# Optimization experiments

Measured on AMD Instinct MI355X. Metric: run time of the kernel, lower is better.

The kernel has to match this reference:

```python
import jax, jax.numpy as jnp
import numpy as np
from jax import lax

D_MODEL = 512
KERNEL = 17
DILATION = 1
MLP_MULT = 4
EPS = 1e-6


def rmsnorm(x, w):
    # x: [B,T,C]; RMSNorm: x * rsqrt(mean(x^2) + eps) * w
    ms = jnp.mean(x * x, axis=-1, keepdims=True)
    return x * lax.rsqrt(ms + EPS) * w


def causal_dwconv(x, w, dilation):
    # x: [B,T,C], w: [C,K]. Equivalent math to the FFT path in the torch code:
    # y[b,t,c] = sum_k w[c,k] * x[b, t - dilation*(K-1) + dilation*k, c] (zeros off left edge)
    B, T, C = x.shape
    K = w.shape[1]
    left_pad = dilation * (K - 1)
    lhs = jnp.transpose(x, (0, 2, 1))          # [B,C,T]
    rhs = w[:, None, :]                        # [C,1,K] depthwise
    y = lax.conv_general_dilated(
        lhs, rhs,
        window_strides=(1,),
        padding=[(left_pad, 0)],
        rhs_dilation=(dilation,),
        dimension_numbers=('NCH', 'OIH', 'NCH'),
        feature_group_count=C,
    )                                          # [B,C,T]
    return jnp.transpose(y, (0, 2, 1))


def setup_inputs() -> dict:
    key = jax.random.key(0)
    ks = jax.random.split(key, 8)
    B, T, d = 4, 16384, D_MODEL
    h = MLP_MULT * d
    scale = lambda fan_in: 1.0 / np.sqrt(fan_in)
    return {
        'x': jax.random.normal(ks[0], (B, T, d), jnp.float32),
        'ln1_w': jnp.ones((d,), jnp.float32),
        'gate_w': jax.random.normal(ks[1], (d, d), jnp.float32) * scale(d),
        'conv_w': jax.random.uniform(ks[2], (d, KERNEL), jnp.float32,
                                     -scale(KERNEL), scale(KERNEL)),
        'proj_w': jax.random.normal(ks[3], (d, d), jnp.float32) * scale(d),
        'ln2_w': jnp.ones((d,), jnp.float32),
        'mlp_w1': jax.random.normal(ks[4], (d, h), jnp.float32) * scale(d),
        'mlp_w2': jax.random.normal(ks[5], (h, d), jnp.float32) * scale(h),
    }


def reference(x, ln1_w, gate_w, conv_w, proj_w, ln2_w, mlp_w1, mlp_w2):
    # Gated depthwise causal conv branch
    hn = rmsnorm(x, ln1_w)
    g = jax.nn.sigmoid(jnp.einsum('btd,de->bte', hn, gate_w))
    hc = causal_dwconv(hn, conv_w, DILATION)
    x = x + jnp.einsum('btd,de->bte', g * hc, proj_w)
    # MLP branch
    hn2 = rmsnorm(x, ln2_w)
    mid = jax.nn.gelu(jnp.einsum('btd,dh->bth', hn2, mlp_w1))
    x = x + jnp.einsum('bth,hd->btd', mid, mlp_w2)
    return x
```

## Files before the change

kernel.cpp:

```cpp
#include <hip/hip_runtime.h>
#include <hip/hip_bf16.h>
#include <cstdint>
#include <cstddef>

typedef __attribute__((ext_vector_type(8))) short short8;
typedef __attribute__((ext_vector_type(4))) short short4v;
typedef __attribute__((ext_vector_type(4))) float floatx4;

#define D_MODEL 512
#define HDIM    2048
#define TSEQ    16384
#define NTOK    65536

__device__ __forceinline__ float bf2f(short s) {
  union { unsigned u; float f; } v; v.u = ((unsigned)(unsigned short)s) << 16; return v.f;
}
__device__ __forceinline__ short f2bf(float f) {
  union { float fv; unsigned u; } v; v.fv = f;
  unsigned u = v.u;
  u += 0x7FFFu + ((u >> 16) & 1u);
  return (short)(u >> 16);
}
__device__ __forceinline__ void gload_lds16(const void* g, void* l) {
  __builtin_amdgcn_global_load_lds((const __attribute__((address_space(1))) void*)g,
                                   (__attribute__((address_space(3))) void*)l, 16, 0, 0);
}

__global__ void wt_transpose(const float* __restrict__ W, short* __restrict__ Wt,
                             const int K, const int N) {
  __shared__ float t[64][65];
  const int tid = threadIdx.x;
  const long k0 = (long)blockIdx.x * 64;
  const long n0 = (long)blockIdx.y * 64;
  const int rr = tid >> 4;
  const int cc = (tid & 15) * 4;
#pragma unroll
  for (int i = 0; i < 4; ++i) {
    const int r = rr + i * 16;
    const float4 v = *(const float4*)(W + (k0 + r) * N + n0 + cc);
    t[r][cc + 0] = v.x; t[r][cc + 1] = v.y; t[r][cc + 2] = v.z; t[r][cc + 3] = v.w;
  }
  __syncthreads();
#pragma unroll
  for (int i = 0; i < 4; ++i) {
    const int n = rr + i * 16;
    short4v o;
    o[0] = f2bf(t[cc + 0][n]);
    o[1] = f2bf(t[cc + 1][n]);
    o[2] = f2bf(t[cc + 2][n]);
    o[3] = f2bf(t[cc + 3][n]);
    *(short4v*)(Wt + (n0 + n) * K + k0 + cc) = o;
  }
}

__global__ void convw_transpose(const float* __restrict__ cw, float* __restrict__ wT) {
  const int idx = blockIdx.x * 256 + threadIdx.x;
  if (idx >= 17 * D_MODEL) return;
  const int k = idx / D_MODEL;
  const int c = idx % D_MODEL;
  wT[idx] = cw[c * 17 + k];
}

__global__ void rmsnorm_kernel(const float* __restrict__ x, const float* __restrict__ w,
                               short* __restrict__ outp) {
  const int lane = threadIdx.x & 63;
  const long row = (long)blockIdx.x * 4 + (threadIdx.x >> 6);
  const float* xr = x + row * D_MODEL + lane * 8;
  const float4 a = *(const float4*)xr;
  const float4 b = *(const float4*)(xr + 4);
  float ss = a.x * a.x + a.y * a.y + a.z * a.z + a.w * a.w
           + b.x * b.x + b.y * b.y + b.z * b.z + b.w * b.w;
#pragma unroll
  for (int m = 32; m; m >>= 1) ss += __shfl_xor(ss, m);
  const float scale = rsqrtf(ss * (1.0f / D_MODEL) + 1e-6f);
  const float4 wa = *(const float4*)(w + lane * 8);
  const float4 wb = *(const float4*)(w + lane * 8 + 4);
  short8 o;
  o[0] = f2bf(a.x * scale * wa.x);
  o[1] = f2bf(a.y * scale * wa.y);
  o[2] = f2bf(a.z * scale * wa.z);
  o[3] = f2bf(a.w * scale * wa.w);
  o[4] = f2bf(b.x * scale * wb.x);
  o[5] = f2bf(b.y * scale * wb.y);
  o[6] = f2bf(b.z * scale * wb.z);
  o[7] = f2bf(b.w * scale * wb.w);
  *(short8*)(outp + row * D_MODEL + lane * 8) = o;
}

__global__ void dwconv_kernel(const short* __restrict__ hn, const float* __restrict__ wT,
                              short* __restrict__ hc) {
  const int tid = threadIdx.x;
  const int chunk = tid & 63;
  const long row = (long)blockIdx.x * 4 + (tid >> 6);
  const int t = (int)(row & (TSEQ - 1));
  const int c0 = chunk * 8;
  float acc[8];
#pragma unroll
  for (int j = 0; j < 8; ++j) acc[j] = 0.f;
  const int kmin = (t >= 16) ? 0 : (16 - t);
  for (int k = kmin; k < 17; ++k) {
    const short8 h = *(const short8*)(hn + (row - 16 + k) * D_MODEL + c0);
    const float* wp = wT + k * D_MODEL + c0;
    const float4 w0 = *(const float4*)(wp);
    const float4 w1 = *(const float4*)(wp + 4);
    acc[0] += bf2f(h[0]) * w0.x;
    acc[1] += bf2f(h[1]) * w0.y;
    acc[2] += bf2f(h[2]) * w0.z;
    acc[3] += bf2f(h[3]) * w0.w;
    acc[4] += bf2f(h[4]) * w1.x;
    acc[5] += bf2f(h[5]) * w1.y;
    acc[6] += bf2f(h[6]) * w1.z;
    acc[7] += bf2f(h[7]) * w1.w;
  }
  short8 o;
#pragma unroll
  for (int j = 0; j < 8; ++j) o[j] = f2bf(acc[j]);
  *(short8*)(hc + row * D_MODEL + c0) = o;
}

#define PHASE_BAR() __builtin_amdgcn_s_barrier()
#define LGKM0() { asm volatile("s_waitcnt lgkmcnt(0)" ::: "memory"); __builtin_amdgcn_sched_barrier(0); }
#define VMC4()  { asm volatile("s_waitcnt vmcnt(4)" ::: "memory"); __builtin_amdgcn_sched_barrier(0); }
#define VMC0()  { asm volatile("s_waitcnt vmcnt(0)" ::: "memory"); __builtin_amdgcn_sched_barrier(0); }
#define DSR1(dst, addr, imm) \
  asm volatile("ds_read_b128 %0, %1 offset:%2" : "=v"(dst) : "v"(addr), "i"(imm))

template <int EPI>
__global__ __launch_bounds__(512, 2)
void gemm256(const short* __restrict__ A, const short* __restrict__ Bt,
             const int K, const int N, const int nbn,
             const void* __restrict__ aux, void* __restrict__ outp) {
  __shared__ short Alds[2 * 2 * 128 * 64];
  __shared__ short Blds[2 * 2 * 128 * 64];
  const int tid = threadIdx.x;
  const int lane = tid & 63;
  const int w = tid >> 6;
  const int wm = w >> 2;
  const int wn = w & 3;

  const int nwg = gridDim.x;
  const int cpx = nwg >> 3;
  const int bid = blockIdx.x;
  const int wid = (bid & 7) * cpx + (bid >> 3);
  const long brow = (long)(wid / nbn) * 256;
  const long bcol = (long)(wid % nbn) * 256;

  floatx4 acc[8][4];
#pragma unroll
  for (int i = 0; i < 8; ++i)
#pragma unroll
    for (int j = 0; j < 4; ++j) acc[i][j] = {0.f, 0.f, 0.f, 0.f};

  short8 af[4][2];
  short8 bfr[4][2];

  const int chunkx = (lane & 7) ^ (lane >> 3);
  const short* gA = A + (brow + w * 8 + (lane >> 3)) * (long)K + chunkx * 8;
  const short* gB = Bt + (bcol + w * 8 + (lane >> 3)) * (long)K + chunkx * 8;
  const int kchunk = lane >> 4;

  const unsigned Abase = (unsigned)(uintptr_t)(__attribute__((address_space(3))) short*)Alds;
  const unsigned Bbase = (unsigned)(uintptr_t)(__attribute__((address_space(3))) short*)Blds;
  const unsigned lanelo = (unsigned)((lane & 15) * 128);
  const unsigned c0t = (unsigned)(((0 + kchunk) ^ (lane & 7)) * 16);
  const unsigned c1t = (unsigned)(((4 + kchunk) ^ (lane & 7)) * 16);
  const unsigned adrA0 = Abase + (unsigned)(wm * 16384) + lanelo + c0t;
  const unsigned adrA1 = Abase + (unsigned)(wm * 16384) + lanelo + c1t;
  const unsigned adrB0 = Bbase + (unsigned)((wn >> 1) * 16384 + (wn & 1) * 8192) + lanelo + c0t;
  const unsigned adrB1 = Bbase + (unsigned)((wn >> 1) * 16384 + (wn & 1) * 8192) + lanelo + c1t;

#define STGA(half, BUF, koff)                                                  \
  { _Pragma("unroll")                                                          \
    for (int j = 0; j < 2; ++j)                                                \
      gload_lds16(gA + ((half) * 128 + j * 64) * (long)K + (koff),             \
                  &Alds[(((BUF) * 2 + (half)) * 128 + j * 64 + w * 8) * 64]); }
#define STGB(half, BUF, koff)                                                  \
  { _Pragma("unroll")                                                          \
    for (int j = 0; j < 2; ++j)                                                \
      gload_lds16(gB + ((half) * 128 + j * 64) * (long)K + (koff),             \
                  &Blds[(((BUF) * 2 + (half)) * 128 + j * 64 + w * 8) * 64]); }

#define LDA4(mbase, BUF) {                                                     \
    DSR1(af[0][0], adrA0, (BUF)*32768 + ((mbase)+0)*2048);                     \
    DSR1(af[0][1], adrA1, (BUF)*32768 + ((mbase)+0)*2048);                     \
    DSR1(af[1][0], adrA0, (BUF)*32768 + ((mbase)+1)*2048);                     \
    DSR1(af[1][1], adrA1, (BUF)*32768 + ((mbase)+1)*2048);                     \
    DSR1(af[2][0], adrA0, (BUF)*32768 + ((mbase)+2)*2048);                     \
    DSR1(af[2][1], adrA1, (BUF)*32768 + ((mbase)+2)*2048);                     \
    DSR1(af[3][0], adrA0, (BUF)*32768 + ((mbase)+3)*2048);                     \
    DSR1(af[3][1], adrA1, (BUF)*32768 + ((mbase)+3)*2048); }
#define LDB2(nbase, BUF) {                                                     \
    DSR1(bfr[(nbase)+0][0], adrB0, (BUF)*32768 + ((nbase)+0)*2048);            \
    DSR1(bfr[(nbase)+0][1], adrB1, (BUF)*32768 + ((nbase)+0)*2048);            \
    DSR1(bfr[(nbase)+1][0], adrB0, (BUF)*32768 + ((nbase)+1)*2048);            \
    DSR1(bfr[(nbase)+1][1], adrB1, (BUF)*32768 + ((nbase)+1)*2048); }

#define MMACL(mbase, nbase)                                                    \
  { __builtin_amdgcn_s_setprio(1);                                             \
    _Pragma("unroll")                                                          \
    for (int mi = 0; mi < 4; ++mi)                                             \
      _Pragma("unroll")                                                        \
      for (int nn = 0; nn < 2; ++nn)                                           \
        _Pragma("unroll")                                                      \
        for (int ks = 0; ks < 2; ++ks)                                         \
          acc[(mbase) + mi][(nbase) + nn] = __builtin_amdgcn_mfma_f32_16x16x32_bf16( \
              af[mi][ks], bfr[(nbase) + nn][ks], acc[(mbase) + mi][(nbase) + nn], 0, 0, 0); \
    __builtin_amdgcn_s_setprio(0); }

#define TILE(BUF, DOST01, DOST23, W4, W0, kA, kB)                              \
  {                                                                            \
                                                                       \
    LDA4(0, BUF); LDB2(0, BUF);                                                \
    if (DOST01) STGA(0, (BUF) ^ 1, kA);                                        \
    PHASE_BAR(); LGKM0(); MMACL(0, 0); PHASE_BAR();                            \
                                                                       \
    LDB2(2, BUF);                                                              \
    if (DOST01) STGA(1, (BUF) ^ 1, kA);                                        \
    PHASE_BAR(); LGKM0(); MMACL(0, 2); PHASE_BAR();                            \
                                                                       \
    LDA4(4, BUF);                                                              \
    if (DOST23) STGB(0, BUF, kB);                                              \
    PHASE_BAR(); LGKM0(); MMACL(4, 0); PHASE_BAR();                            \
                                                                       \
    if (DOST23) STGB(1, BUF, kB);                                              \
    PHASE_BAR(); MMACL(4, 2);                                                  \
    if (W4) VMC4();                                                            \
    if (W0) VMC0();                                                            \
    PHASE_BAR();                                                               \
  }

  STGB(0, 0, 0); STGB(1, 0, 0); STGA(0, 0, 0); STGA(1, 0, 0);
  STGB(0, 1, 64); STGB(1, 1, 64);
  VMC4(); PHASE_BAR();

  const int nkt = K >> 6;
  int kA = 64, kB = 128;
  for (int t = 0; t < nkt - 2; t += 2) {
    TILE(0, 1, 1, 1, 0, kA, kB); kA += 64; kB += 64;
    TILE(1, 1, 1, 1, 0, kA, kB); kA += 64; kB += 64;
  }
  TILE(0, 1, 0, 0, 1, kA, 0);
  TILE(1, 0, 0, 0, 0, 0, 0);

#undef TILE
#undef MMACL
#undef LDA4
#undef LDB2
#undef STGA
#undef STGB

#pragma unroll
  for (int mi = 0; mi < 8; ++mi) {
    const int r0 = (int)brow + wm * 128 + mi * 16 + (lane >> 4) * 4;
#pragma unroll
    for (int j = 0; j < 4; ++j) {
      const int rb = (r0 + j) * N;
      const int gcb = (int)bcol + wn * 64 + (lane & 15);
#pragma unroll
      for (int ni = 0; ni < 4; ++ni) {
        const int idx = rb + gcb + ni * 16;
        const float v = acc[mi][ni][j];
        if (EPI == 0) {
          const float hcv = bf2f(((const short*)aux)[idx]);
          const float g = 1.f / (1.f + __expf(-v));
          ((short*)outp)[idx] = f2bf(g * hcv);
        } else if (EPI == 1) {
          ((float*)outp)[idx] = ((const float*)aux)[idx] + v;
        } else if (EPI == 2) {
          const float x3 = v * v * v;
          const float z = 0.7978845608028654f * (v + 0.044715f * x3);
          const float th = 1.f - 2.f / (__expf(2.f * z) + 1.f);
          ((short*)outp)[idx] = f2bf(0.5f * v * (1.f + th));
        } else {
          ((float*)outp)[idx] += v;
        }
      }
    }
  }
}

extern "C" void kernel_launch(void* const* d_in, const int* in_sizes, int n_in,
                              void* d_out, int out_size, void* d_ws, size_t ws_size,
                              hipStream_t stream) {
  const float* x      = (const float*)d_in[0];
  const float* ln1_w  = (const float*)d_in[1];
  const float* gate_w = (const float*)d_in[2];
  const float* conv_w = (const float*)d_in[3];
  const float* proj_w = (const float*)d_in[4];
  const float* ln2_w  = (const float*)d_in[5];
  const float* mlp_w1 = (const float*)d_in[6];
  const float* mlp_w2 = (const float*)d_in[7];
  float* out = (float*)d_out;
  char* ws = (char*)d_ws;

  short* hn      = (short*)(ws + 0);
  short* hc      = (short*)(ws + 67108864L);
  short* mid     = (short*)(ws + 134217728L);
  short* gate_wt = (short*)(ws + 402653184L);
  short* proj_wt = (short*)(ws + 403177472L);
  short* w1t     = (short*)(ws + 403701760L);
  short* w2t     = (short*)(ws + 405798912L);
  float* convwT  = (float*)(ws + 407896064L);

  const dim3 b256(256);
  const dim3 b512(512);

  wt_transpose<<<dim3(8, 8),  b256, 0, stream>>>(gate_w, gate_wt, 512, 512);
  wt_transpose<<<dim3(8, 8),  b256, 0, stream>>>(proj_w, proj_wt, 512, 512);
  wt_transpose<<<dim3(8, 32), b256, 0, stream>>>(mlp_w1, w1t, 512, 2048);
  wt_transpose<<<dim3(32, 8), b256, 0, stream>>>(mlp_w2, w2t, 2048, 512);
  convw_transpose<<<34, b256, 0, stream>>>(conv_w, convwT);

  rmsnorm_kernel<<<NTOK / 4, b256, 0, stream>>>(x, ln1_w, hn);
  dwconv_kernel<<<NTOK / 4, b256, 0, stream>>>(hn, convwT, hc);
  gemm256<0><<<256 * 2, b512, 0, stream>>>(hn, gate_wt, 512, 512, 2, hc, hc);
  gemm256<1><<<256 * 2, b512, 0, stream>>>(hc, proj_wt, 512, 512, 2, x, out);
  rmsnorm_kernel<<<NTOK / 4, b256, 0, stream>>>(out, ln2_w, hn);
  gemm256<2><<<256 * 8, b512, 0, stream>>>(hn, w1t, 512, 2048, 8, nullptr, mid);
  gemm256<3><<<256 * 2, b512, 0, stream>>>(mid, w2t, 2048, 512, 2, nullptr, out);
}
```

Before: 695.9 us.

## Switch GEMM inner loop to 32x32x16 bf16 MFMA tiles

Replaces the 16x16x32 MFMA tiling with 32x32x16 MFMAs, reshaping the per-wave accumulators into 4x2 blocks of 16-float vectors and reworking the LDS fragment addressing and reads to match. The larger MFMA shape cuts the number of LDS fragment reads per FLOP and the count of MFMA instructions issued. It also adds a partial lgkmcnt wait before the first barrier. The epilogue index mapping is rewritten for the 32x32 output layout, which risks wrong results if the swizzle or row mapping is off, and register pressure changes with 2 waves per SIMD.

After: 805.9 us. +15.8%, slower.

```diff
diff --git a/kernel.cpp b/kernel.cpp
--- a/kernel.cpp
+++ b/kernel.cpp
@@ -5,7 +5,7 @@
 
 typedef __attribute__((ext_vector_type(8))) short short8;
 typedef __attribute__((ext_vector_type(4))) short short4v;
-typedef __attribute__((ext_vector_type(4))) float floatx4;
+typedef __attribute__((ext_vector_type(16))) float floatx16;
 
 #define D_MODEL 512
 #define HDIM    2048
@@ -120,6 +120,7 @@
 
 #define PHASE_BAR() __builtin_amdgcn_s_barrier()
 #define LGKM0() { asm volatile("s_waitcnt lgkmcnt(0)" ::: "memory"); __builtin_amdgcn_sched_barrier(0); }
+#define LGKM4() { asm volatile("s_waitcnt lgkmcnt(4)" ::: "memory"); __builtin_amdgcn_sched_barrier(0); }
 #define VMC4()  { asm volatile("s_waitcnt vmcnt(4)" ::: "memory"); __builtin_amdgcn_sched_barrier(0); }
 #define VMC0()  { asm volatile("s_waitcnt vmcnt(0)" ::: "memory"); __builtin_amdgcn_sched_barrier(0); }
 #define DSR1(dst, addr, imm) \
@@ -145,29 +146,34 @@
   const long brow = (long)(wid / nbn) * 256;
   const long bcol = (long)(wid % nbn) * 256;
 
-  floatx4 acc[8][4];
-#pragma unroll
-  for (int i = 0; i < 8; ++i)
-#pragma unroll
-    for (int j = 0; j < 4; ++j) acc[i][j] = {0.f, 0.f, 0.f, 0.f};
-
-  short8 af[4][2];
-  short8 bfr[4][2];
+  floatx16 acc[4][2];
+#pragma unroll
+  for (int i = 0; i < 4; ++i)
+#pragma unroll
+    for (int j = 0; j < 2; ++j)
+#pragma unroll
+      for (int e = 0; e < 16; ++e) acc[i][j][e] = 0.f;
+
+  short8 af[2][4];
+  short8 bfr[2][4];
 
   const int chunkx = (lane & 7) ^ (lane >> 3);
   const short* gA = A + (brow + w * 8 + (lane >> 3)) * (long)K + chunkx * 8;
   const short* gB = Bt + (bcol + w * 8 + (lane >> 3)) * (long)K + chunkx * 8;
-  const int kchunk = lane >> 4;
 
   const unsigned Abase = (unsigned)(uintptr_t)(__attribute__((address_space(3))) short*)Alds;
   const unsigned Bbase = (unsigned)(uintptr_t)(__attribute__((address_space(3))) short*)Blds;
-  const unsigned lanelo = (unsigned)((lane & 15) * 128);
-  const unsigned c0t = (unsigned)(((0 + kchunk) ^ (lane & 7)) * 16);
-  const unsigned c1t = (unsigned)(((4 + kchunk) ^ (lane & 7)) * 16);
-  const unsigned adrA0 = Abase + (unsigned)(wm * 16384) + lanelo + c0t;
-  const unsigned adrA1 = Abase + (unsigned)(wm * 16384) + lanelo + c1t;
-  const unsigned adrB0 = Bbase + (unsigned)((wn >> 1) * 16384 + (wn & 1) * 8192) + lanelo + c0t;
-  const unsigned adrB1 = Bbase + (unsigned)((wn >> 1) * 16384 + (wn & 1) * 8192) + lanelo + c1t;
+  const unsigned lane31 = (unsigned)((lane & 31) * 128);
+  const unsigned khi = (unsigned)(lane >> 5);
+  const unsigned lxor = (unsigned)(lane & 7);
+  const unsigned c0t = ((0u * 2 + khi) ^ lxor) * 16;
+  const unsigned c1t = ((1u * 2 + khi) ^ lxor) * 16;
+  const unsigned c2t = ((2u * 2 + khi) ^ lxor) * 16;
+  const unsigned c3t = ((3u * 2 + khi) ^ lxor) * 16;
+  const unsigned aoff = Abase + (unsigned)(wm * 16384) + lane31;
+  const unsigned boff = Bbase + (unsigned)((wn >> 1) * 16384 + (wn & 1) * 8192) + lane31;
+  const unsigned adrA0 = aoff + c0t, adrA1 = aoff + c1t, adrA2 = aoff + c2t, adrA3 = aoff + c3t;
+  const unsigned adrB0 = boff + c0t, adrB1 = boff + c1t, adrB2 = boff + c2t, adrB3 = boff + c3t;
 
 #define STGA(half, BUF, koff)                                                  \
   { _Pragma("unroll")                                                          \
@@ -180,50 +186,49 @@
       gload_lds16(gB + ((half) * 128 + j * 64) * (long)K + (koff),             \
                   &Blds[(((BUF) * 2 + (half)) * 128 + j * 64 + w * 8) * 64]); }
 
-#define LDA4(mbase, BUF) {                                                     \
-    DSR1(af[0][0], adrA0, (BUF)*32768 + ((mbase)+0)*2048);                     \
-    DSR1(af[0][1], adrA1, (BUF)*32768 + ((mbase)+0)*2048);                     \
-    DSR1(af[1][0], adrA0, (BUF)*32768 + ((mbase)+1)*2048);                     \
-    DSR1(af[1][1], adrA1, (BUF)*32768 + ((mbase)+1)*2048);                     \
-    DSR1(af[2][0], adrA0, (BUF)*32768 + ((mbase)+2)*2048);                     \
-    DSR1(af[2][1], adrA1, (BUF)*32768 + ((mbase)+2)*2048);                     \
-    DSR1(af[3][0], adrA0, (BUF)*32768 + ((mbase)+3)*2048);                     \
-    DSR1(af[3][1], adrA1, (BUF)*32768 + ((mbase)+3)*2048); }
-#define LDB2(nbase, BUF) {                                                     \
-    DSR1(bfr[(nbase)+0][0], adrB0, (BUF)*32768 + ((nbase)+0)*2048);            \
-    DSR1(bfr[(nbase)+0][1], adrB1, (BUF)*32768 + ((nbase)+0)*2048);            \
-    DSR1(bfr[(nbase)+1][0], adrB0, (BUF)*32768 + ((nbase)+1)*2048);            \
-    DSR1(bfr[(nbase)+1][1], adrB1, (BUF)*32768 + ((nbase)+1)*2048); }
-
-#define MMACL(mbase, nbase)                                                    \
+#define LDA32(mbase, BUF) {                                                    \
+    DSR1(af[0][0], adrA0, (BUF)*32768 + ((mbase)+0)*4096);                     \
+    DSR1(af[0][1], adrA1, (BUF)*32768 + ((mbase)+0)*4096);                     \
+    DSR1(af[0][2], adrA2, (BUF)*32768 + ((mbase)+0)*4096);                     \
+    DSR1(af[0][3], adrA3, (BUF)*32768 + ((mbase)+0)*4096);                     \
+    DSR1(af[1][0], adrA0, (BUF)*32768 + ((mbase)+1)*4096);                     \
+    DSR1(af[1][1], adrA1, (BUF)*32768 + ((mbase)+1)*4096);                     \
+    DSR1(af[1][2], adrA2, (BUF)*32768 + ((mbase)+1)*4096);                     \
+    DSR1(af[1][3], adrA3, (BUF)*32768 + ((mbase)+1)*4096); }
+#define LDB32(nb, BUF) {                                                       \
+    DSR1(bfr[nb][0], adrB0, (BUF)*32768 + (nb)*4096);                          \
+    DSR1(bfr[nb][1], adrB1, (BUF)*32768 + (nb)*4096);                          \
+    DSR1(bfr[nb][2], adrB2, (BUF)*32768 + (nb)*4096);                          \
+    DSR1(bfr[nb][3], adrB3, (BUF)*32768 + (nb)*4096); }
+
+#define MMACL32(mbase, nb)                                                     \
   { __builtin_amdgcn_s_setprio(1);                                             \
     _Pragma("unroll")                                                          \
-    for (int mi = 0; mi < 4; ++mi)                                             \
+    for (int i = 0; i < 2; ++i)                                                \
       _Pragma("unroll")                                                        \
-      for (int nn = 0; nn < 2; ++nn)                                           \
-        _Pragma("unroll")                                                      \
-        for (int ks = 0; ks < 2; ++ks)                                         \
-          acc[(mbase) + mi][(nbase) + nn] = __builtin_amdgcn_mfma_f32_16x16x32_bf16( \
-              af[mi][ks], bfr[(nbase) + nn][ks], acc[(mbase) + mi][(nbase) + nn], 0, 0, 0); \
+      for (int ks = 0; ks < 4; ++ks)                                           \
+        acc[(mbase) + i][nb] = __builtin_amdgcn_mfma_f32_32x32x16_bf16(        \
+            af[i][ks], bfr[nb][ks], acc[(mbase) + i][nb], 0, 0, 0);            \
     __builtin_amdgcn_s_setprio(0); }
 
 #define TILE(BUF, DOST01, DOST23, W4, W0, kA, kB)                              \
   {                                                                            \
-                                                                       \
-    LDA4(0, BUF); LDB2(0, BUF);                                                \
+                                             \
+    LDA32(0, BUF); LDB32(0, BUF);                                              \
     if (DOST01) STGA(0, (BUF) ^ 1, kA);                                        \
-    PHASE_BAR(); LGKM0(); MMACL(0, 0); PHASE_BAR();                            \
-                                                                       \
-    LDB2(2, BUF);                                                              \
+    LGKM4();                                                                   \
+    PHASE_BAR(); LGKM0(); MMACL32(0, 0); PHASE_BAR();                          \
+                                                          \
+    LDB32(1, BUF);                                                             \
     if (DOST01) STGA(1, (BUF) ^ 1, kA);                                        \
-    PHASE_BAR(); LGKM0(); MMACL(0, 2); PHASE_BAR();                            \
-                                                                       \
-    LDA4(4, BUF);                                                              \
+    PHASE_BAR(); LGKM0(); MMACL32(0, 1); PHASE_BAR();                          \
+                                                          \
+    LDA32(2, BUF);                                                             \
     if (DOST23) STGB(0, BUF, kB);                                              \
-    PHASE_BAR(); LGKM0(); MMACL(4, 0); PHASE_BAR();                            \
-                                                                       \
+    PHASE_BAR(); LGKM0(); MMACL32(2, 0); PHASE_BAR();                          \
+                                                          \
     if (DOST23) STGB(1, BUF, kB);                                              \
-    PHASE_BAR(); MMACL(4, 2);                                                  \
+    PHASE_BAR(); MMACL32(2, 1);                                                \
     if (W4) VMC4();                                                            \
     if (W0) VMC0();                                                            \
     PHASE_BAR();                                                               \
@@ -243,23 +248,23 @@
   TILE(1, 0, 0, 0, 0, 0, 0);
 
 #undef TILE
-#undef MMACL
-#undef LDA4
-#undef LDB2
+#undef MMACL32
+#undef LDA32
+#undef LDB32
 #undef STGA
 #undef STGB
 
 #pragma unroll
-  for (int mi = 0; mi < 8; ++mi) {
-    const int r0 = (int)brow + wm * 128 + mi * 16 + (lane >> 4) * 4;
-#pragma unroll
-    for (int j = 0; j < 4; ++j) {
-      const int rb = (r0 + j) * N;
-      const int gcb = (int)bcol + wn * 64 + (lane & 15);
-#pragma unroll
-      for (int ni = 0; ni < 4; ++ni) {
-        const int idx = rb + gcb + ni * 16;
-        const float v = acc[mi][ni][j];
+  for (int mb = 0; mb < 4; ++mb) {
+#pragma unroll
+    for (int nb = 0; nb < 2; ++nb) {
+      const int col = (int)bcol + wn * 64 + nb * 32 + (lane & 31);
+      const int rbase = (int)brow + wm * 128 + mb * 32 + ((lane >> 5) << 2);
+#pragma unroll
+      for (int reg = 0; reg < 16; ++reg) {
+        const int row = rbase + (reg & 3) + ((reg >> 2) << 3);
+        const int idx = row * N + col;
+        const float v = acc[mb][nb][reg];
         if (EPI == 0) {
           const float hcv = bf2f(((const short*)aux)[idx]);
           const float g = 1.f / (1.f + __expf(-v));
```
